# Kernel optimization log

Measured on AMD Instinct MI355X. Metric: run time of the kernel, lower is better.

## Reference

```python
import jax, jax.numpy as jnp
import numpy as np

B, D, K = 16384, 32, 128  # batch, cluster_dim, num_clusters


def setup_inputs() -> dict:
    key = jax.random.key(0)
    x = jax.random.normal(key, (B, D, K), dtype=jnp.float32)
    mu_0 = jnp.zeros((D, K), dtype=jnp.float32)                      # running mean buffer
    L_0 = jnp.broadcast_to(jnp.eye(D, dtype=jnp.float32), (K, D, D)) # running Cholesky buffer
    n_0 = jnp.ones((1,), dtype=jnp.float32)                          # running count
    return {"x": x, "mu_0": mu_0, "L_0": L_0, "n_0": n_0}


def reference(x, mu_0, L_0, n_0):
    # Training-mode forward of ClusterNorm1dv2.
    Bn = x.shape[0]
    eps_eye = jnp.eye(x.shape[1], dtype=x.dtype)
    n0 = n_0[0]
    x_mu = jnp.mean(x, axis=0)                         # [D, K]
    x_cnt = jnp.transpose(x - x_mu[None], (2, 1, 0))   # [K, D, B]
    C = jnp.einsum('kdb,keb->kde', x_cnt, x_cnt)       # [K, D, D] per-cluster scatter
    denom = n0 + Bn
    new_mu = (n0 * mu_0 + Bn * x_mu) / denom           # [D, K]
    x_d = jnp.transpose((x_mu - mu_0)[None], (2, 1, 0))  # [K, D, 1]
    new_cov = (jnp.einsum('kde,kfe->kdf', L_0, L_0) * (n0 / denom)
               + C / denom
               + jnp.einsum('kdo,keo->kde', x_d, x_d) * (n0 * Bn / denom ** 2))
    L = jnp.linalg.cholesky(new_cov + eps_eye)         # [K, D, D]
    xc = jnp.transpose(x - new_mu[None], (2, 1, 0))    # [K, D, B]
    Z = jax.scipy.linalg.solve_triangular(L, xc, lower=True)  # whitening solve
    return jnp.transpose(Z, (2, 1, 0))                 # [B, D, K]
```

## Files before the change

### kernel.cpp

```cpp
#include <hip/hip_runtime.h>

typedef __attribute__((ext_vector_type(4))) float f32x4;

#define NB 16384
#define ND 32
#define NK 128

template<int SP>
__device__ __forceinline__ void k1_body(const float* __restrict__ x,
                                        float* __restrict__ part,
                                        float* __restrict__ vs,
                                        int k0, int b0, int t) {
  constexpr int CL = 4*(SP+1);
  constexpr int CH = 4*(8-SP);
  const int sd = t >> 3, sj = t & 7;
  const int kl = t & 63;

  float aL[4][CL];
  float aH[4][CH];
  float ssum[8];
  #pragma unroll
  for (int r=0;r<4;r++){
    #pragma unroll
    for (int c=0;c<CL;c++) aL[r][c]=0.f;
    #pragma unroll
    for (int c=0;c<CH;c++) aH[r][c]=0.f;
  }
  #pragma unroll
  for (int i=0;i<8;i++) ssum[i]=0.f;

  for (int g=0; g<32; ++g) {
    #pragma unroll
    for (int s=0;s<2;s++){
      const int b = b0 + g*2 + s;
      const float* src = x + ((size_t)b*ND + sd)*NK + k0 + 4*sj;
      const f32x4 A0 = *(const f32x4*)src;
      const f32x4 A1 = *(const f32x4*)(src+32);
      float* dst = vs + s*2304;
      #pragma unroll
      for (int i=0;i<4;i++){
        dst[(4*sj+i)*36 + sd]    = A0[i];
        dst[(4*sj+32+i)*36 + sd] = A1[i];
        ssum[i]   += A0[i];
        ssum[4+i] += A1[i];
      }
    }
    __syncthreads();
    #pragma unroll
    for (int s=0;s<2;s++){
      const float* row = vs + s*2304 + kl*36;
      f32x4 bv[8-SP];
      #pragma unroll
      for (int q=0;q<8-SP;q++) bv[q] = *(const f32x4*)(row + 4*q);
      #pragma unroll
      for (int r=0;r<4;r++){
        const float al = bv[SP][r];
        const float ah = bv[7-SP][r];
        #pragma unroll
        for (int q=0;q<=SP;q++){
          #pragma unroll
          for (int i=0;i<4;i++) aL[r][4*q+i] += al*bv[q][i];
        }
        #pragma unroll
        for (int q=0;q<8-SP;q++){
          #pragma unroll
          for (int i=0;i<4;i++) aH[r][4*q+i] += ah*bv[q][i];
        }
      }
    }
    __syncthreads();
  }

  float* pb = part + (size_t)blockIdx.x*38912;
  #pragma unroll
  for (int r=0;r<4;r++){
    #pragma unroll
    for (int c=0;c<CL;c++)
      __builtin_nontemporal_store(aL[r][c], &pb[(8*SP*(SP+1) + r*CL + c)*64 + kl]);
    #pragma unroll
    for (int c=0;c<CH;c++)
      __builtin_nontemporal_store(aH[r][c], &pb[(8*(7-SP)*(8-SP) + r*CH + c)*64 + kl]);
  }
  #pragma unroll
  for (int i=0;i<4;i++){
    __builtin_nontemporal_store(ssum[i],   &pb[(576+sd)*64 + 4*sj + i]);
    __builtin_nontemporal_store(ssum[4+i], &pb[(576+sd)*64 + 32 + 4*sj + i]);
  }
}

__global__ __launch_bounds__(256, 2) void k1_scatter(const float* __restrict__ x,
                                                     float* __restrict__ part) {
  __shared__ float vs[2*2304];
  const int t = threadIdx.x;
  const int ktile = blockIdx.x & 1;
  const int chunk = blockIdx.x >> 1;
  const int k0 = ktile*64, b0 = chunk*64;
  switch (t>>6) {
    case 0:  k1_body<0>(x, part, vs, k0, b0, t); break;
    case 1:  k1_body<1>(x, part, vs, k0, b0, t); break;
    case 2:  k1_body<2>(x, part, vs, k0, b0, t); break;
    default: k1_body<3>(x, part, vs, k0, b0, t); break;
  }
}

__global__ void k2a_reduce(const float* __restrict__ part, float* __restrict__ sfin) {
  const int t = threadIdx.x;
  const int bx = blockIdx.x;
  const int h = bx & 1, ktile = (bx>>1)&1, vg = bx>>2;
  const int vidx = vg*4 + (t>>6);
  const int kl = t & 63;
  const float* p = part + ((size_t)(h*128)*2 + ktile)*38912 + vidx*64 + kl;
  float a0=0.f,a1=0.f,a2=0.f,a3=0.f;
  for (int c=0;c<128;c+=4){
    a0 += __builtin_nontemporal_load(&p[(size_t)(c+0)*77824]);
    a1 += __builtin_nontemporal_load(&p[(size_t)(c+1)*77824]);
    a2 += __builtin_nontemporal_load(&p[(size_t)(c+2)*77824]);
    a3 += __builtin_nontemporal_load(&p[(size_t)(c+3)*77824]);
  }
  sfin[h*77824 + vidx*128 + ktile*64 + kl] = (a0+a1)+(a2+a3);
}

__global__ void k2b_chol(const float* __restrict__ sfin,
                         const float* __restrict__ mu0,
                         const float* __restrict__ L0,
                         const float* __restrict__ n0p,
                         float* __restrict__ lpad,
                         float* __restrict__ nmu) {
  const int k = blockIdx.x;
  const int t = threadIdx.x;
  __shared__ float L0s[32*33];
  __shared__ float Am[32*33];
  __shared__ float xdl[32];
  __shared__ float dinv[32];
  const float n0 = n0p[0];
  const float denom = n0 + (float)NB;

  for (int idx = t; idx < 1024; idx += 256)
    L0s[(idx>>5)*33 + (idx&31)] = L0[k*1024 + idx];
  if (t < 32) {
    const float S  = sfin[(576+t)*128 + k] + sfin[77824 + (576+t)*128 + k];
    const float m0 = mu0[t*128 + k];
    nmu[t*128 + k] = (n0*m0 + S) / denom;
    xdl[t] = S*(1.0f/NB) - m0;
  }
  __syncthreads();

  const float c1 = n0/denom, c2 = 1.0f/denom;
  const float c3 = n0*(float)NB/(denom*denom);
  for (int idx = t; idx < 1024; idx += 256) {
    const int d = idx>>5, e = idx&31;
    const int dd = d>=e?d:e, ee = d>=e?e:d;
    const int R = dd>>2;
    const int vi = 8*R*(R+1) + (dd&3)*4*(R+1) + ee;
    const float M  = sfin[vi*128 + k]      + sfin[77824 + vi*128 + k];
    const float Sd = sfin[(576+d)*128 + k] + sfin[77824 + (576+d)*128 + k];
    const float Se = sfin[(576+e)*128 + k] + sfin[77824 + (576+e)*128 + k];
    const float C = M - Sd*Se*(1.0f/NB);
    float g = 0.f;
    #pragma unroll 8
    for (int f=0; f<32; f++) g += L0s[d*33+f]*L0s[e*33+f];
    float a = g*c1 + C*c2 + xdl[d]*xdl[e]*c3;
    if (d==e) a += 1.0f;
    Am[d*33+e] = a;
  }
  __syncthreads();

  for (int j=0;j<32;j++){
    float acc = 0.f;
    if (t < 32 && t >= j) {
      acc = Am[t*33+j];
      for (int e=0;e<j;e++) acc -= Am[t*33+e]*Am[j*33+e];
    }
    __syncthreads();
    if (t == j) {
      const float dj = sqrtf(acc);
      Am[j*33+j] = dj;
      dinv[j] = 1.0f/dj;
    }
    __syncthreads();
    if (t < 32 && t > j) Am[t*33+j] = acc*dinv[j];
    __syncthreads();
  }

  if (t < 32) {
    const int d = t;
    int rs = 0;
    for (int e=0;e<d;e++) rs += (e+3)>>2;
    rs *= 4;
    const int rl = ((d+3)>>2)*4;
    float* lp = lpad + k*576;
    for (int e=0;e<rl;e++) lp[rs+e] = (e<d) ? Am[d*33+e] : 0.f;
    lp[544+d] = dinv[d];
  }
}

__global__ __launch_bounds__(256, 2) void k3_whiten(const float* __restrict__ x,
                                                    const float* __restrict__ lpad,
                                                    const float* __restrict__ nmu,
                                                    float* __restrict__ out) {
  __shared__ float Lw[32*580];
  __shared__ float muL[32*32];
  const int t = threadIdx.x;
  const int bx = blockIdx.x;
  const int m = (bx >> 3) & 1;
  const int u = ((bx >> 4) << 3) | (bx & 7);
  const int ktile = ((u & 1) << 1) | m;
  const int chunk = u >> 1;
  const int k0 = ktile*32;

  {
    const f32x4* src = (const f32x4*)(lpad + (size_t)k0*576);
    #pragma unroll
    for (int q=0;q<18;q++){
      const int idx = t + q*256;
      const int row = idx/144, col = idx - row*144;
      *(f32x4*)(&Lw[row*580 + col*4]) = src[idx];
    }
    #pragma unroll
    for (int idx=t; idx<1024; idx+=256)
      muL[idx] = nmu[(idx>>5)*128 + k0 + (idx&31)];
  }
  __syncthreads();

  const int kl = t & 31;
  const int so = t >> 5;
  const float* Lrow = &Lw[kl*580];
  const int b0 = chunk*128;

  for (int it=0; it<4; ++it) {
    const int base = b0 + it*32 + so;
    const float* xa = x + (size_t)(base     )*4096 + k0 + kl;
    const float* xb = x + (size_t)(base +  8)*4096 + k0 + kl;
    const float* xc = x + (size_t)(base + 16)*4096 + k0 + kl;
    const float* xd = x + (size_t)(base + 24)*4096 + k0 + kl;
    float vA[32], vB[32], vC[32], vD[32];
    #pragma unroll
    for (int d=0; d<32; ++d) vA[d] = xa[d*128];
    #pragma unroll
    for (int d=0; d<32; ++d) vB[d] = xb[d*128];
    #pragma unroll
    for (int d=0; d<32; ++d) vC[d] = xc[d*128];
    #pragma unroll
    for (int d=0; d<32; ++d) vD[d] = xd[d*128];
    #pragma unroll
    for (int d=0; d<32; ++d) {
      const float m2 = muL[d*32 + kl];
      vA[d] -= m2; vB[d] -= m2; vC[d] -= m2; vD[d] -= m2;
    }
    int rs = 0;
    #pragma unroll
    for (int d=0; d<32; ++d) {
      float sA = vA[d], sB = vB[d], sC = vC[d], sD = vD[d];
      const int nq = (d+3)>>2;
      #pragma unroll
      for (int q=0; q<nq; ++q) {
        const f32x4 Lq = *(const f32x4*)(Lrow + rs + 4*q);
        sA -= Lq[0]*vA[4*q+0] + Lq[1]*vA[4*q+1] + Lq[2]*vA[4*q+2] + Lq[3]*vA[4*q+3];
        sB -= Lq[0]*vB[4*q+0] + Lq[1]*vB[4*q+1] + Lq[2]*vB[4*q+2] + Lq[3]*vB[4*q+3];
        sC -= Lq[0]*vC[4*q+0] + Lq[1]*vC[4*q+1] + Lq[2]*vC[4*q+2] + Lq[3]*vC[4*q+3];
        sD -= Lq[0]*vD[4*q+0] + Lq[1]*vD[4*q+1] + Lq[2]*vD[4*q+2] + Lq[3]*vD[4*q+3];
      }
      const float di = Lrow[544+d];
      vA[d] = sA*di; vB[d] = sB*di; vC[d] = sC*di; vD[d] = sD*di;
      rs += 4*nq;
    }
    float* oa = out + (size_t)(base     )*4096 + k0 + kl;
    float* ob = out + (size_t)(base +  8)*4096 + k0 + kl;
    float* oc = out + (size_t)(base + 16)*4096 + k0 + kl;
    float* od = out + (size_t)(base + 24)*4096 + k0 + kl;
    #pragma unroll
    for (int d=0; d<32; ++d) __builtin_nontemporal_store(vA[d], oa + d*128);
    #pragma unroll
    for (int d=0; d<32; ++d) __builtin_nontemporal_store(vB[d], ob + d*128);
    #pragma unroll
    for (int d=0; d<32; ++d) __builtin_nontemporal_store(vC[d], oc + d*128);
    #pragma unroll
    for (int d=0; d<32; ++d) __builtin_nontemporal_store(vD[d], od + d*128);
  }
}

extern "C" void kernel_launch(void* const* d_in, const int* in_sizes, int n_in,
                              void* d_out, int out_size, void* d_ws, size_t ws_size,
                              hipStream_t stream) {
  const float* x   = (const float*)d_in[0];
  const float* mu0 = (const float*)d_in[1];
  const float* L0  = (const float*)d_in[2];
  const float* n0  = (const float*)d_in[3];
  float* out  = (float*)d_out;
  float* part = out;
  float* sfin = out + 20971520;
  float* lpad = (float*)d_ws;
  float* nmu  = lpad + 128*576;

  k1_scatter<<<512, 256, 0, stream>>>(x, part);
  k2a_reduce<<<608, 256, 0, stream>>>(part, sfin);
  k2b_chol  <<<128, 256, 0, stream>>>(sfin, mu0, L0, n0, lpad, nmu);
  k3_whiten <<<512, 256, 0, stream>>>(x, lpad, nmu, out);
}
```

Measured before the change: 203.7 us.

## Split scatter accumulation across 512 threads with paired rows per wave

The scatter kernel now runs 512 threads per block, so each of 8 waves owns two low and two high triangle rows (balanced pairs) instead of 4-row bands. Global loads are split so each half of the block stages one of the two batch samples, and the column sums are computed from shared memory per owned row rather than at load time. This cuts per-thread accumulator registers and raises the number of waves available to hide latency, at the cost of more shared-memory reads per FMA and a launch-bounds change to 512x4.

```diff
diff --git a/kernel.cpp b/kernel.cpp
--- a/kernel.cpp
+++ b/kernel.cpp
@@ -5,67 +5,66 @@
 #define NB 16384
 #define ND 32
 #define NK 128
+
+__host__ __device__ constexpr int rbase(int d) {
+  return 8*(d>>2)*((d>>2)+1) + (d&3)*4*((d>>2)+1);
+}
 
 template<int SP>
 __device__ __forceinline__ void k1_body(const float* __restrict__ x,
                                         float* __restrict__ part,
                                         float* __restrict__ vs,
                                         int k0, int b0, int t) {
-  constexpr int CL = 4*(SP+1);
-  constexpr int CH = 4*(8-SP);
-  const int sd = t >> 3, sj = t & 7;
+  constexpr int RL0 = 2*SP,    RL1 = 2*SP+1;
+  constexpr int RH0 = 30-2*SP, RH1 = 31-2*SP;
+  constexpr int CL  = 4*(RL1>>2)+4;
+  constexpr int CH  = 4*(RH1>>2)+4;
+  constexpr int NG  = CH/4;
+  constexpr int GLO = RL0>>2, GHI = RH0>>2;
+
   const int kl = t & 63;
-
-  float aL[4][CL];
-  float aH[4][CH];
-  float ssum[8];
-  #pragma unroll
-  for (int r=0;r<4;r++){
-    #pragma unroll
-    for (int c=0;c<CL;c++) aL[r][c]=0.f;
-    #pragma unroll
-    for (int c=0;c<CH;c++) aH[r][c]=0.f;
-  }
-  #pragma unroll
-  for (int i=0;i<8;i++) ssum[i]=0.f;
+  const int ss = t >> 8, sd = (t & 255) >> 3, sj = t & 7;
+
+  float aL0[CL], aL1[CL], aH0[CH], aH1[CH];
+  float ssum[4];
+  #pragma unroll
+  for (int c=0;c<CL;c++){ aL0[c]=0.f; aL1[c]=0.f; }
+  #pragma unroll
+  for (int c=0;c<CH;c++){ aH0[c]=0.f; aH1[c]=0.f; }
+  #pragma unroll
+  for (int i=0;i<4;i++) ssum[i]=0.f;
 
   for (int g=0; g<32; ++g) {
-    #pragma unroll
-    for (int s=0;s<2;s++){
-      const int b = b0 + g*2 + s;
-      const float* src = x + ((size_t)b*ND + sd)*NK + k0 + 4*sj;
+    {
+      const float* src = x + ((size_t)(b0 + 2*g + ss)*ND + sd)*NK + k0 + 4*sj;
       const f32x4 A0 = *(const f32x4*)src;
       const f32x4 A1 = *(const f32x4*)(src+32);
-      float* dst = vs + s*2304;
+      float* dst = vs + ss*2304;
       #pragma unroll
       for (int i=0;i<4;i++){
-        dst[(4*sj+i)*36 + sd]    = A0[i];
-        dst[(4*sj+32+i)*36 + sd] = A1[i];
-        ssum[i]   += A0[i];
-        ssum[4+i] += A1[i];
+        dst[(4*sj+i)*36 + sd]      = A0[i];
+        dst[(4*(sj+8)+i)*36 + sd]  = A1[i];
       }
     }
     __syncthreads();
     #pragma unroll
     for (int s=0;s<2;s++){
       const float* row = vs + s*2304 + kl*36;
-      f32x4 bv[8-SP];
+      const f32x4 glo = *(const f32x4*)(row + 4*GLO);
+      const f32x4 ghi = *(const f32x4*)(row + 4*GHI);
+      const float dL0 = glo[RL0&3], dL1 = glo[RL1&3];
+      const float dH0 = ghi[RH0&3], dH1 = ghi[RH1&3];
+      ssum[0]+=dL0; ssum[1]+=dL1; ssum[2]+=dH0; ssum[3]+=dH1;
       #pragma unroll
-      for (int q=0;q<8-SP;q++) bv[q] = *(const f32x4*)(row + 4*q);
-      #pragma unroll
-      for (int r=0;r<4;r++){
-        const float al = bv[SP][r];
-        const float ah = bv[7-SP][r];
-        #pragma unroll
-        for (int q=0;q<=SP;q++){
+      for (int q=0;q<NG;q++){
+        const f32x4 vq = (q==GLO) ? glo : (q==GHI) ? ghi
+                         : *(const f32x4*)(row + 4*q);
+        if (4*q < CL) {
           #pragma unroll
-          for (int i=0;i<4;i++) aL[r][4*q+i] += al*bv[q][i];
+          for (int i=0;i<4;i++){ aL0[4*q+i]+=dL0*vq[i]; aL1[4*q+i]+=dL1*vq[i]; }
         }
         #pragma unroll
-        for (int q=0;q<8-SP;q++){
-          #pragma unroll
-          for (int i=0;i<4;i++) aH[r][4*q+i] += ah*bv[q][i];
-        }
+        for (int i=0;i<4;i++){ aH0[4*q+i]+=dH0*vq[i]; aH1[4*q+i]+=dH1*vq[i]; }
       }
     }
     __syncthreads();
@@ -73,22 +72,22 @@
 
   float* pb = part + (size_t)blockIdx.x*38912;
   #pragma unroll
-  for (int r=0;r<4;r++){
-    #pragma unroll
-    for (int c=0;c<CL;c++)
-      __builtin_nontemporal_store(aL[r][c], &pb[(8*SP*(SP+1) + r*CL + c)*64 + kl]);
-    #pragma unroll
-    for (int c=0;c<CH;c++)
-      __builtin_nontemporal_store(aH[r][c], &pb[(8*(7-SP)*(8-SP) + r*CH + c)*64 + kl]);
-  }
-  #pragma unroll
-  for (int i=0;i<4;i++){
-    __builtin_nontemporal_store(ssum[i],   &pb[(576+sd)*64 + 4*sj + i]);
-    __builtin_nontemporal_store(ssum[4+i], &pb[(576+sd)*64 + 32 + 4*sj + i]);
-  }
-}
-
-__global__ __launch_bounds__(256, 2) void k1_scatter(const float* __restrict__ x,
+  for (int c=0;c<CL;c++){
+    __builtin_nontemporal_store(aL0[c], &pb[(rbase(RL0)+c)*64 + kl]);
+    __builtin_nontemporal_store(aL1[c], &pb[(rbase(RL1)+c)*64 + kl]);
+  }
+  #pragma unroll
+  for (int c=0;c<CH;c++){
+    __builtin_nontemporal_store(aH0[c], &pb[(rbase(RH0)+c)*64 + kl]);
+    __builtin_nontemporal_store(aH1[c], &pb[(rbase(RH1)+c)*64 + kl]);
+  }
+  __builtin_nontemporal_store(ssum[0], &pb[(576+RL0)*64 + kl]);
+  __builtin_nontemporal_store(ssum[1], &pb[(576+RL1)*64 + kl]);
+  __builtin_nontemporal_store(ssum[2], &pb[(576+RH0)*64 + kl]);
+  __builtin_nontemporal_store(ssum[3], &pb[(576+RH1)*64 + kl]);
+}
+
+__global__ __launch_bounds__(512, 4) void k1_scatter(const float* __restrict__ x,
                                                      float* __restrict__ part) {
   __shared__ float vs[2*2304];
   const int t = threadIdx.x;
@@ -99,7 +98,11 @@
     case 0:  k1_body<0>(x, part, vs, k0, b0, t); break;
     case 1:  k1_body<1>(x, part, vs, k0, b0, t); break;
     case 2:  k1_body<2>(x, part, vs, k0, b0, t); break;
-    default: k1_body<3>(x, part, vs, k0, b0, t); break;
+    case 3:  k1_body<3>(x, part, vs, k0, b0, t); break;
+    case 4:  k1_body<4>(x, part, vs, k0, b0, t); break;
+    case 5:  k1_body<5>(x, part, vs, k0, b0, t); break;
+    case 6:  k1_body<6>(x, part, vs, k0, b0, t); break;
+    default: k1_body<7>(x, part, vs, k0, b0, t); break;
   }
 }
 
@@ -150,8 +153,7 @@
   for (int idx = t; idx < 1024; idx += 256) {
     const int d = idx>>5, e = idx&31;
     const int dd = d>=e?d:e, ee = d>=e?e:d;
-    const int R = dd>>2;
-    const int vi = 8*R*(R+1) + (dd&3)*4*(R+1) + ee;
+    const int vi = rbase(dd) + ee;
     const float M  = sfin[vi*128 + k]      + sfin[77824 + vi*128 + k];
     const float Sd = sfin[(576+d)*128 + k] + sfin[77824 + (576+d)*128 + k];
     const float Se = sfin[(576+e)*128 + k] + sfin[77824 + (576+e)*128 + k];
@@ -292,7 +294,7 @@
   float* lpad = (float*)d_ws;
   float* nmu  = lpad + 128*576;
 
-  k1_scatter<<<512, 256, 0, stream>>>(x, part);
+  k1_scatter<<<512, 512, 0, stream>>>(x, part);
   k2a_reduce<<<608, 256, 0, stream>>>(part, sfin);
   k2b_chol  <<<128, 256, 0, stream>>>(sfin, mu0, L0, n0, lpad, nmu);
   k3_whiten <<<512, 256, 0, stream>>>(x, lpad, nmu, out);
```

Result: slower. 211.8 us (+4.0%).
